# Kernel tuning notes

Hardware: AMD Instinct MI355X
Metric: run time of the kernel (lower is better)

## Reference

```python
import jax, jax.numpy as jnp
import numpy as np

B, S, D, H = 4, 1024, 2048, 16
DH = D // H          # head_dim = 128
EPS = 1e-6           # equinox nn.RMSNorm default eps


def setup_inputs() -> dict:
    ks = jax.random.split(jax.random.key(0), 8)
    return {
        "x": jax.random.normal(ks[0], (B, S, D), jnp.float32),
        # Flux-style rope table, broadcast over heads: (B, S, 1, d_head/2, 2, 2)
        "pe": jax.random.normal(ks[1], (B, S, 1, DH // 2, 2, 2), jnp.float32),
        "w_qkv": jax.random.normal(ks[2], (D, 3 * D), jnp.float32) * (1.0 / np.sqrt(D)),
        "w_o": jax.random.normal(ks[3], (D, D), jnp.float32) * (1.0 / np.sqrt(D)),
        "q_scale": 1.0 + 0.02 * jax.random.normal(ks[4], (DH,), jnp.float32),
        "q_bias": 0.02 * jax.random.normal(ks[5], (DH,), jnp.float32),
        "k_scale": 1.0 + 0.02 * jax.random.normal(ks[6], (DH,), jnp.float32),
        "k_bias": 0.02 * jax.random.normal(ks[7], (DH,), jnp.float32),
    }


def reference(x, pe, w_qkv, w_o, q_scale, q_bias, k_scale, k_bias):
    b, s, dm = x.shape
    # fused QKV projection -> (B, S, 3, H, DH); rearrange '(qkv heads dim)'
    qkv = (x @ w_qkv).reshape(b, s, 3, H, DH)
    q, k, v = qkv[:, :, 0], qkv[:, :, 1], qkv[:, :, 2]

    # per-head RMSNorm (QKNorm), eqx: w * (x / rms) + b
    def rms(u, scale, bias):
        inv = jax.lax.rsqrt(jnp.mean(u * u, axis=-1, keepdims=True) + EPS)
        return u * inv * scale + bias

    q = rms(q, q_scale, q_bias)
    k = rms(k, k_scale, k_bias)

    # RoPE: view last dim as (DH//2, 1, 2) pairs, apply 2x2 rotation from pe
    def rope(u):
        u2 = u.reshape(b, s, H, DH // 2, 1, 2)
        r = pe[..., 0] * u2[..., 0] + pe[..., 1] * u2[..., 1]  # (B,S,H,DH//2,2)
        return r.reshape(b, s, H, DH)

    q = rope(q)
    k = rope(k)

    # non-causal SDPA, layout (B, T, N, H), default scale 1/sqrt(DH)
    attn = jax.nn.dot_product_attention(q, k, v)
    return attn.reshape(b, s, dm) @ w_o
```

## Files before the change

kernel.cpp:

```cpp
#include <hip/hip_runtime.h>
#include <hip/hip_bf16.h>

typedef _Float16 f16_t;
typedef _Float16 f16x2 __attribute__((ext_vector_type(2)));
typedef _Float16 f16x4 __attribute__((ext_vector_type(4)));
typedef _Float16 f16x8 __attribute__((ext_vector_type(8)));
typedef float f32x4 __attribute__((ext_vector_type(4)));

#define GLOAD_LDS16(gp, lp)                                                        \
  __builtin_amdgcn_global_load_lds(                                                \
      (const __attribute__((address_space(1))) void*)(gp),                         \
      (__attribute__((address_space(3))) void*)(lp), 16, 0, 0)

template<int N> __device__ __forceinline__ void vmwait() {
    if constexpr (N == 0)      asm volatile("s_waitcnt vmcnt(0)" ::: "memory");
    else if constexpr (N == 3) asm volatile("s_waitcnt vmcnt(3)" ::: "memory");
    else if constexpr (N == 5) asm volatile("s_waitcnt vmcnt(5)" ::: "memory");
    else if constexpr (N == 6) asm volatile("s_waitcnt vmcnt(6)" ::: "memory");
    else                       asm volatile("s_waitcnt vmcnt(0)" ::: "memory");
}

__global__ __launch_bounds__(256) void conv_f16(const float* __restrict__ in,
                                                f16_t* __restrict__ out)
{
    int i = blockIdx.x * 256 + threadIdx.x;
    float4 a = *(const float4*)&in[(size_t)i * 8];
    float4 b = *(const float4*)&in[(size_t)i * 8 + 4];
    f16x8 o = {(f16_t)a.x, (f16_t)a.y, (f16_t)a.z, (f16_t)a.w,
               (f16_t)b.x, (f16_t)b.y, (f16_t)b.z, (f16_t)b.w};
    *(f16x8*)&out[(size_t)i * 8] = o;
}

__global__ __launch_bounds__(256) void transpose_f16(const float* __restrict__ in,
                                                     f16_t* __restrict__ out,
                                                     int R, int C)
{
    __shared__ float t[32][33];
    const int tr = blockIdx.y, tc = blockIdx.x;
    const int r = threadIdx.x >> 3, c4 = (threadIdx.x & 7) * 4;
    float4 v = *(const float4*)&in[(size_t)(tr * 32 + r) * C + tc * 32 + c4];
    t[r][c4 + 0] = v.x; t[r][c4 + 1] = v.y; t[r][c4 + 2] = v.z; t[r][c4 + 3] = v.w;
    __syncthreads();
    f16x4 o = {(f16_t)t[c4 + 0][r], (f16_t)t[c4 + 1][r],
               (f16_t)t[c4 + 2][r], (f16_t)t[c4 + 3][r]};
    *(f16x4*)&out[(size_t)(tc * 32 + r) * R + tr * 32 + c4] = o;
}

template<int BM, int BN, int GY, int F16OUT>
__global__ __launch_bounds__(512, 2) void gemm_v4(const f16_t* __restrict__ A,
                                                  const f16_t* __restrict__ BT,
                                                  void* __restrict__ Cout,
                                                  int M, int N, int K)
{
    extern __shared__ char smem[];
    constexpr int WMT = BM / 2, WNT = BN / 4;
    constexpr int MF = WMT / 16, NF = WNT / 16, MFH = MF / 2, NFH = NF / 2;
    constexpr int ALI = BM / 128, BLI = BN / 128;
    constexpr int L = ALI + BLI;
    constexpr int ABUFB = BM * 64, BBUFB = BN * 64;

    const int tid = threadIdx.x, lane = tid & 63, wave = tid >> 6;
    const int lh = lane >> 4, li = lane & 15;
    const int wr = wave >> 2, wc = wave & 3;

    const int nwg = gridDim.x, bid = blockIdx.x;
    const int swz = (bid & 7) * (nwg >> 3) + (bid >> 3);
    const int by = swz % GY, bx = swz / GY;

    const size_t bmK = (size_t)(by * BM) * K;
    const size_t bnK = (size_t)(bx * BN) * K;
    const int NT = K >> 5;

    f32x4 acc[MF][NF];
#pragma unroll
    for (int i = 0; i < MF; ++i)
#pragma unroll
        for (int j = 0; j < NF; ++j) acc[i][j] = (f32x4){0.f, 0.f, 0.f, 0.f};

#define STAGE(t, b)                                                                \
    do {                                                                           \
        const int kof_ = (t) << 5;                                                 \
        char* Ab_ = smem + (b) * ABUFB;                                            \
        char* Bb_ = smem + 3 * ABUFB + (b) * BBUFB;                                \
        _Pragma("unroll")                                                          \
        for (int i_ = 0; i_ < ALI; ++i_) {                                         \
            const int c_ = i_ * 512 + tid;                                         \
            const int row_ = c_ >> 2;                                              \
            const int gu_ = (c_ & 3) ^ ((row_ >> 1) & 3);                          \
            GLOAD_LDS16(A + bmK + (size_t)row_ * K + kof_ + gu_ * 8,               \
                        Ab_ + (i_ * 512 + wave * 64) * 16);                        \
        }                                                                          \
        _Pragma("unroll")                                                          \
        for (int i_ = 0; i_ < BLI; ++i_) {                                         \
            const int c_ = i_ * 512 + tid;                                         \
            const int row_ = c_ >> 2;                                              \
            const int gu_ = (c_ & 3) ^ ((row_ >> 1) & 3);                          \
            GLOAD_LDS16(BT + bnK + (size_t)row_ * K + kof_ + gu_ * 8,              \
                        Bb_ + (i_ * 512 + wave * 64) * 16);                        \
        }                                                                          \
    } while (0)

    STAGE(0, 0);
    STAGE(1, 1);

    const int runit = (lh ^ ((li >> 1) & 3)) << 3;

    int rb = 0;
    for (int t = 0; t < NT; ++t) {
        if (t + 1 < NT) vmwait<L>();
        else            vmwait<0>();
        __builtin_amdgcn_s_barrier();
        __builtin_amdgcn_sched_barrier(0);

        if (t + 2 < NT) {
            const int sb = rb ? rb - 1 : 2;
            STAGE(t + 2, sb);
        }

        const f16_t* Ab = (const f16_t*)(smem + rb * ABUFB);
        const f16_t* Bb = (const f16_t*)(smem + 3 * ABUFB + rb * BBUFB);

        f16x8 af[2][MFH], bf[NFH];
#pragma unroll
        for (int ah = 0; ah < 2; ++ah)
#pragma unroll
            for (int j = 0; j < MFH; ++j)
                af[ah][j] = *(const f16x8*)(Ab + (wr * WMT + (ah * MFH + j) * 16 + li) * 32
                                            + runit);
#pragma unroll
        for (int j = 0; j < NFH; ++j)
            bf[j] = *(const f16x8*)(Bb + (wc * WNT + j * 16 + li) * 32 + runit);

        __builtin_amdgcn_s_setprio(1);
#pragma unroll
        for (int ah = 0; ah < 2; ++ah)
#pragma unroll
            for (int i = 0; i < MFH; ++i)
#pragma unroll
                for (int j = 0; j < NFH; ++j)
                    acc[ah * MFH + i][j] = __builtin_amdgcn_mfma_f32_16x16x32_f16(
                        af[ah][i], bf[j], acc[ah * MFH + i][j], 0, 0, 0);
        __builtin_amdgcn_s_setprio(0);

#pragma unroll
        for (int j = 0; j < NFH; ++j)
            bf[j] = *(const f16x8*)(Bb + (wc * WNT + (NFH + j) * 16 + li) * 32 + runit);

        __builtin_amdgcn_s_setprio(1);
#pragma unroll
        for (int ah = 0; ah < 2; ++ah)
#pragma unroll
            for (int i = 0; i < MFH; ++i)
#pragma unroll
                for (int j = 0; j < NFH; ++j)
                    acc[ah * MFH + i][NFH + j] = __builtin_amdgcn_mfma_f32_16x16x32_f16(
                        af[ah][i], bf[j], acc[ah * MFH + i][NFH + j], 0, 0, 0);
        __builtin_amdgcn_s_setprio(0);

        __builtin_amdgcn_sched_barrier(0);
        rb = (rb == 2) ? 0 : rb + 1;
    }
#undef STAGE

#pragma unroll
    for (int mf = 0; mf < MF; ++mf)
#pragma unroll
        for (int nf = 0; nf < NF; ++nf)
#pragma unroll
            for (int r = 0; r < 4; ++r) {
                const int row = by * BM + wr * WMT + mf * 16 + lh * 4 + r;
                const int col = bx * BN + wc * WNT + nf * 16 + li;
                if (F16OUT)
                    ((f16_t*)Cout)[(size_t)row * N + col] = (f16_t)acc[mf][nf][r];
                else
                    ((float*)Cout)[(size_t)row * N + col] = acc[mf][nf][r];
            }
}

__global__ __launch_bounds__(256) void rmsrope_f16(f16_t* __restrict__ qkv,
                                                   const float* __restrict__ pe,
                                                   const float* __restrict__ qs,
                                                   const float* __restrict__ qb,
                                                   const float* __restrict__ ks,
                                                   const float* __restrict__ kb)
{
    const int unit = blockIdx.x * 4 + (threadIdx.x >> 6);
    const int l = threadIdx.x & 63;
    const int bs = unit >> 5, h = (unit >> 1) & 15, comp = unit & 1;
    f16_t* base = qkv + ((size_t)bs * 3 + comp) * 2048 + h * 128;
    const float* sc = comp ? ks : qs;
    const float* bi = comp ? kb : qb;

    f16x2 u = *(const f16x2*)(base + 2 * l);
    float u0 = (float)u[0], u1 = (float)u[1];
    float ss = u0 * u0 + u1 * u1;
#pragma unroll
    for (int o = 32; o; o >>= 1) ss += __shfl_xor(ss, o);
    float inv = rsqrtf(ss * (1.f / 128.f) + 1e-6f);

    float2 scv = *(const float2*)(sc + 2 * l);
    float2 biv = *(const float2*)(bi + 2 * l);
    float a = u0 * inv * scv.x + biv.x;
    float c = u1 * inv * scv.y + biv.y;
    float4 p4 = *(const float4*)(pe + (size_t)bs * 256 + l * 4);
    f16x2 o = {(f16_t)(p4.x * a + p4.y * c), (f16_t)(p4.z * a + p4.w * c)};
    *(f16x2*)(base + 2 * l) = o;
}

__global__ __launch_bounds__(256) void attn_f16(const f16_t* __restrict__ qkv,
                                                f16_t* __restrict__ out)
{
    __shared__ f16_t Kl[2][64 * 128];
    __shared__ f16_t Vt[128 * 72];
    const int tid = threadIdx.x, lane = tid & 63, wave = tid >> 6;
    const int lh = lane >> 4, li = lane & 15;
    const int bidx = blockIdx.x;
    const int bh = bidx & 63;
    const int qt = bidx >> 6;
    const int h = bh & 15, b = bh >> 4;
    const size_t seqbase = (size_t)b * 1024;
    const float SCALE = 0.08838834764831845f;

    const int qbase = qt * 128 + wave * 32;
    f16x8 qreg[2][4];
#pragma unroll
    for (int qf = 0; qf < 2; ++qf) {
        const f16_t* qp = qkv + (seqbase + qbase + qf * 16 + li) * 6144 + h * 128;
#pragma unroll
        for (int c = 0; c < 4; ++c) {
            f16x8 v = *(const f16x8*)(qp + c * 32 + lh * 8);
#pragma unroll
            for (int j = 0; j < 8; ++j) v[j] = (f16_t)((float)v[j] * SCALE);
            qreg[qf][c] = v;
        }
    }

    f32x4 oacc[2][8];
#pragma unroll
    for (int qf = 0; qf < 2; ++qf)
#pragma unroll
        for (int dt = 0; dt < 8; ++dt) oacc[qf][dt] = (f32x4){0.f, 0.f, 0.f, 0.f};
    float mrun[2] = {-1e30f, -1e30f}, lrun[2] = {0.f, 0.f};

    const int vd0 = (tid & 31) * 4;
    const int vk0 = (tid >> 5) * 8;
    f16x4 vreg[8];

#define STAGE_K(t, buf)                                                            \
    do {                                                                           \
        _Pragma("unroll")                                                          \
        for (int it = 0; it < 4; ++it) {                                           \
            const int c_ = it * 256 + tid;                                         \
            const int row_ = c_ >> 4, cc_ = c_ & 15;                               \
            const f16_t* src_ = qkv + (seqbase + (t) * 64 + row_) * 6144 + 2048 +  \
                                h * 128 + ((cc_ ^ (row_ & 7)) << 3);               \
            GLOAD_LDS16(src_, (char*)&Kl[buf][0] + (it * 256 + wave * 64) * 16);   \
        }                                                                          \
    } while (0)

#define LOAD_V(t)                                                                  \
    do {                                                                           \
        _Pragma("unroll")                                                          \
        for (int r_ = 0; r_ < 8; ++r_)                                             \
            vreg[r_] = *(const f16x4*)(qkv + (seqbase + (t) * 64 + vk0 + r_) *     \
                                       6144 + 4096 + h * 128 + vd0);               \
    } while (0)

    STAGE_K(0, 0);
    LOAD_V(0);

    for (int t = 0; t < 16; ++t) {
        const int buf = t & 1;
        __syncthreads();

#pragma unroll
        for (int dd = 0; dd < 4; ++dd) {
            f16x8 w;
#pragma unroll
            for (int r = 0; r < 8; ++r) w[r] = vreg[r][dd];
            *(f16x8*)&Vt[(vd0 + dd) * 72 + vk0] = w;
        }
        __syncthreads();

        if (t < 15) {
            STAGE_K(t + 1, buf ^ 1);
            LOAD_V(t + 1);
        }

        float s[2][16];
#pragma unroll
        for (int kvt = 0; kvt < 4; ++kvt) {
            f32x4 a0 = (f32x4){0.f, 0.f, 0.f, 0.f}, a1 = a0;
#pragma unroll
            for (int c = 0; c < 4; ++c) {
                const int kvrow = kvt * 16 + li;
                f16x8 kf = *(const f16x8*)&Kl[buf][kvrow * 128 +
                                                   (((c * 4 + lh) ^ (li & 7)) << 3)];
                a0 = __builtin_amdgcn_mfma_f32_16x16x32_f16(kf, qreg[0][c], a0, 0, 0, 0);
                a1 = __builtin_amdgcn_mfma_f32_16x16x32_f16(kf, qreg[1][c], a1, 0, 0, 0);
            }
#pragma unroll
            for (int r = 0; r < 4; ++r) { s[0][kvt * 4 + r] = a0[r]; s[1][kvt * 4 + r] = a1[r]; }
        }

        float pmax[2];
#pragma unroll
        for (int qf = 0; qf < 2; ++qf) {
            float mx = s[qf][0];
#pragma unroll
            for (int i = 1; i < 16; ++i) mx = fmaxf(mx, s[qf][i]);
            mx = fmaxf(mx, __shfl_xor(mx, 16));
            mx = fmaxf(mx, __shfl_xor(mx, 32));
            pmax[qf] = mx;
        }
        const bool defer = __all((pmax[0] - mrun[0] <= 8.f) && (pmax[1] - mrun[1] <= 8.f));
        if (!defer) {
#pragma unroll
            for (int qf = 0; qf < 2; ++qf) {
                const float mn = fmaxf(mrun[qf], pmax[qf]);
                const float alpha = __expf(mrun[qf] - mn);
                lrun[qf] *= alpha;
                mrun[qf] = mn;
                float ar[4];
#pragma unroll
                for (int r = 0; r < 4; ++r) ar[r] = __shfl(alpha, 4 * lh + r);
#pragma unroll
                for (int dt = 0; dt < 8; ++dt)
#pragma unroll
                    for (int r = 0; r < 4; ++r) oacc[qf][dt][r] *= ar[r];
            }
        }

        f16x8 pa[2][2];
#pragma unroll
        for (int qf = 0; qf < 2; ++qf) {
            float ls = 0.f;
            float p[16];
#pragma unroll
            for (int i = 0; i < 16; ++i) { p[i] = __expf(s[qf][i] - mrun[qf]); ls += p[i]; }
            ls += __shfl_xor(ls, 16);
            ls += __shfl_xor(ls, 32);
            lrun[qf] += ls;
#pragma unroll
            for (int hf = 0; hf < 2; ++hf)
#pragma unroll
                for (int j = 0; j < 8; ++j)
                    pa[qf][hf][j] = (f16_t)p[(2 * hf + (j >> 2)) * 4 + (j & 3)];
        }

#pragma unroll
        for (int dt = 0; dt < 8; ++dt) {
            const int drow = dt * 16 + li;
            f16x4 v0 = *(const f16x4*)&Vt[drow * 72 + 4 * lh];
            f16x4 v1 = *(const f16x4*)&Vt[drow * 72 + 16 + 4 * lh];
            f16x4 v2 = *(const f16x4*)&Vt[drow * 72 + 32 + 4 * lh];
            f16x4 v3 = *(const f16x4*)&Vt[drow * 72 + 48 + 4 * lh];
            f16x8 vf0 = {v0[0], v0[1], v0[2], v0[3], v1[0], v1[1], v1[2], v1[3]};
            f16x8 vf1 = {v2[0], v2[1], v2[2], v2[3], v3[0], v3[1], v3[2], v3[3]};
#pragma unroll
            for (int qf = 0; qf < 2; ++qf) {
                oacc[qf][dt] = __builtin_amdgcn_mfma_f32_16x16x32_f16(pa[qf][0], vf0,
                                                                      oacc[qf][dt], 0, 0, 0);
                oacc[qf][dt] = __builtin_amdgcn_mfma_f32_16x16x32_f16(pa[qf][1], vf1,
                                                                      oacc[qf][dt], 0, 0, 0);
            }
        }
    }

#pragma unroll
    for (int qf = 0; qf < 2; ++qf) {
        const float inv = 1.f / lrun[qf];
        float ir[4];
#pragma unroll
        for (int r = 0; r < 4; ++r) ir[r] = __shfl(inv, 4 * lh + r);
#pragma unroll
        for (int dt = 0; dt < 8; ++dt)
#pragma unroll
            for (int r = 0; r < 4; ++r) {
                const int row = qbase + qf * 16 + 4 * lh + r;
                out[(seqbase + row) * 2048 + h * 128 + dt * 16 + li] =
                    (f16_t)(oacc[qf][dt][r] * ir[r]);
            }
    }
#undef STAGE_K
#undef LOAD_V
}

extern "C" void kernel_launch(void* const* d_in, const int* in_sizes, int n_in,
                              void* d_out, int out_size, void* d_ws, size_t ws_size,
                              hipStream_t stream) {
    const float* x       = (const float*)d_in[0];
    const float* pe      = (const float*)d_in[1];
    const float* w_qkv   = (const float*)d_in[2];
    const float* w_o     = (const float*)d_in[3];
    const float* q_scale = (const float*)d_in[4];
    const float* q_bias  = (const float*)d_in[5];
    const float* k_scale = (const float*)d_in[6];
    const float* k_bias  = (const float*)d_in[7];
    float* out = (float*)d_out;

    char* ws = (char*)d_ws;
    f16_t* x16    = (f16_t*)(ws);
    f16_t* wqkvT  = (f16_t*)(ws + 16777216);
    f16_t* woT    = (f16_t*)(ws + 41943040);
    f16_t* qkv16  = (f16_t*)(ws + 50331648);
    f16_t* attn16 = (f16_t*)(ws + 100663296);

    hipFuncSetAttribute((const void*)&gemm_v4<256, 384, 16, 1>,
                        hipFuncAttributeMaxDynamicSharedMemorySize, 122880);
    hipFuncSetAttribute((const void*)&gemm_v4<128, 256, 32, 0>,
                        hipFuncAttributeMaxDynamicSharedMemorySize, 73728);

    conv_f16<<<4096, 256, 0, stream>>>(x, x16);
    transpose_f16<<<dim3(6144 / 32, 2048 / 32), 256, 0, stream>>>(w_qkv, wqkvT, 2048, 6144);
    transpose_f16<<<dim3(2048 / 32, 2048 / 32), 256, 0, stream>>>(w_o, woT, 2048, 2048);

    gemm_v4<256, 384, 16, 1><<<256, 512, 122880, stream>>>(x16, wqkvT, qkv16,
                                                           4096, 6144, 2048);

    rmsrope_f16<<<32768, 256, 0, stream>>>(qkv16, pe, q_scale, q_bias, k_scale, k_bias);

    attn_f16<<<512, 256, 0, stream>>>(qkv16, attn16);

    gemm_v4<128, 256, 32, 0><<<256, 512, 73728, stream>>>(attn16, woT, out,
                                                          4096, 2048, 2048);
}
```

Measured before the change: 273.8 us.

## Split GEMM main loop into four barrier-synced phases interleaving LDS reads and staging

Restructures the GEMM k-loop into four MFMA phases separated by workgroup barriers, interleaving LDS fragment reads with split A/B global-to-LDS staging so memory issue and matrix math from different waves overlap in a ping-pong style. The wait for the next tile moves to the end of the iteration, with a prologue wait before the loop. This adds three extra barriers per k-step in exchange for better overlap. Buffer reuse safety relies on the three-buffer rotation and barrier placement.

```diff
diff --git a/kernel.cpp b/kernel.cpp
--- a/kernel.cpp
+++ b/kernel.cpp
@@ -16,9 +16,15 @@
     if constexpr (N == 0)      asm volatile("s_waitcnt vmcnt(0)" ::: "memory");
     else if constexpr (N == 3) asm volatile("s_waitcnt vmcnt(3)" ::: "memory");
     else if constexpr (N == 5) asm volatile("s_waitcnt vmcnt(5)" ::: "memory");
-    else if constexpr (N == 6) asm volatile("s_waitcnt vmcnt(6)" ::: "memory");
     else                       asm volatile("s_waitcnt vmcnt(0)" ::: "memory");
 }
+
+#define PHASE_SYNC()                                                               \
+    do {                                                                           \
+        __builtin_amdgcn_s_barrier();                                              \
+        asm volatile("s_waitcnt lgkmcnt(0)" ::: "memory");                         \
+        __builtin_amdgcn_sched_barrier(0);                                         \
+    } while (0)
 
 __global__ __launch_bounds__(256) void conv_f16(const float* __restrict__ in,
                                                 f16_t* __restrict__ out)
@@ -47,7 +53,7 @@
 }
 
 template<int BM, int BN, int GY, int F16OUT>
-__global__ __launch_bounds__(512, 2) void gemm_v4(const f16_t* __restrict__ A,
+__global__ __launch_bounds__(512, 2) void gemm_v7(const f16_t* __restrict__ A,
                                                   const f16_t* __restrict__ BT,
                                                   void* __restrict__ Cout,
                                                   int M, int N, int K)
@@ -77,11 +83,10 @@
 #pragma unroll
         for (int j = 0; j < NF; ++j) acc[i][j] = (f32x4){0.f, 0.f, 0.f, 0.f};
 
-#define STAGE(t, b)                                                                \
+#define STAGE_A(t, b)                                                              \
     do {                                                                           \
         const int kof_ = (t) << 5;                                                 \
         char* Ab_ = smem + (b) * ABUFB;                                            \
-        char* Bb_ = smem + 3 * ABUFB + (b) * BBUFB;                                \
         _Pragma("unroll")                                                          \
         for (int i_ = 0; i_ < ALI; ++i_) {                                         \
             const int c_ = i_ * 512 + tid;                                         \
@@ -90,6 +95,12 @@
             GLOAD_LDS16(A + bmK + (size_t)row_ * K + kof_ + gu_ * 8,               \
                         Ab_ + (i_ * 512 + wave * 64) * 16);                        \
         }                                                                          \
+    } while (0)
+
+#define STAGE_B(t, b)                                                              \
+    do {                                                                           \
+        const int kof_ = (t) << 5;                                                 \
+        char* Bb_ = smem + 3 * ABUFB + (b) * BBUFB;                                \
         _Pragma("unroll")                                                          \
         for (int i_ = 0; i_ < BLI; ++i_) {                                         \
             const int c_ = i_ * 512 + tid;                                         \
@@ -100,67 +111,85 @@
         }                                                                          \
     } while (0)
 
-    STAGE(0, 0);
-    STAGE(1, 1);
+    STAGE_A(0, 0); STAGE_B(0, 0);
+    STAGE_A(1, 1); STAGE_B(1, 1);
+    vmwait<L>();
+    __builtin_amdgcn_s_barrier();
+    __builtin_amdgcn_sched_barrier(0);
 
     const int runit = (lh ^ ((li >> 1) & 3)) << 3;
 
     int rb = 0;
     for (int t = 0; t < NT; ++t) {
-        if (t + 1 < NT) vmwait<L>();
-        else            vmwait<0>();
+        const f16_t* Ab = (const f16_t*)(smem + rb * ABUFB);
+        const f16_t* Bb = (const f16_t*)(smem + 3 * ABUFB + rb * BBUFB);
+        const int sb = rb ? rb - 1 : 2;
+        const bool stg = (t + 2 < NT);
+
+        f16x8 af[2][MFH], bf[NFH];
+
+#pragma unroll
+        for (int j = 0; j < MFH; ++j)
+            af[0][j] = *(const f16x8*)(Ab + (wr * WMT + j * 16 + li) * 32 + runit);
+#pragma unroll
+        for (int j = 0; j < NFH; ++j)
+            bf[j] = *(const f16x8*)(Bb + (wc * WNT + j * 16 + li) * 32 + runit);
+        if (stg) STAGE_A(t + 2, sb);
+        PHASE_SYNC();
+        __builtin_amdgcn_s_setprio(1);
+#pragma unroll
+        for (int i = 0; i < MFH; ++i)
+#pragma unroll
+            for (int j = 0; j < NFH; ++j)
+                acc[i][j] = __builtin_amdgcn_mfma_f32_16x16x32_f16(af[0][i], bf[j],
+                                                                   acc[i][j], 0, 0, 0);
+        __builtin_amdgcn_s_setprio(0);
+
+#pragma unroll
+        for (int j = 0; j < MFH; ++j)
+            af[1][j] = *(const f16x8*)(Ab + (wr * WMT + (MFH + j) * 16 + li) * 32 + runit);
+        if (stg) STAGE_B(t + 2, sb);
+        PHASE_SYNC();
+        __builtin_amdgcn_s_setprio(1);
+#pragma unroll
+        for (int i = 0; i < MFH; ++i)
+#pragma unroll
+            for (int j = 0; j < NFH; ++j)
+                acc[MFH + i][j] = __builtin_amdgcn_mfma_f32_16x16x32_f16(af[1][i], bf[j],
+                                                                         acc[MFH + i][j],
+                                                                         0, 0, 0);
+        __builtin_amdgcn_s_setprio(0);
+
+#pragma unroll
+        for (int j = 0; j < NFH; ++j)
+            bf[j] = *(const f16x8*)(Bb + (wc * WNT + (NFH + j) * 16 + li) * 32 + runit);
+        PHASE_SYNC();
+        __builtin_amdgcn_s_setprio(1);
+#pragma unroll
+        for (int i = 0; i < MFH; ++i)
+#pragma unroll
+            for (int j = 0; j < NFH; ++j)
+                acc[MFH + i][NFH + j] = __builtin_amdgcn_mfma_f32_16x16x32_f16(
+                    af[1][i], bf[j], acc[MFH + i][NFH + j], 0, 0, 0);
+        __builtin_amdgcn_s_setprio(0);
+
+        if (stg) vmwait<L>();
+        else     vmwait<0>();
         __builtin_amdgcn_s_barrier();
         __builtin_amdgcn_sched_barrier(0);
-
-        if (t + 2 < NT) {
-            const int sb = rb ? rb - 1 : 2;
-            STAGE(t + 2, sb);
-        }
-
-        const f16_t* Ab = (const f16_t*)(smem + rb * ABUFB);
-        const f16_t* Bb = (const f16_t*)(smem + 3 * ABUFB + rb * BBUFB);
-
-        f16x8 af[2][MFH], bf[NFH];
-#pragma unroll
-        for (int ah = 0; ah < 2; ++ah)
-#pragma unroll
-            for (int j = 0; j < MFH; ++j)
-                af[ah][j] = *(const f16x8*)(Ab + (wr * WMT + (ah * MFH + j) * 16 + li) * 32
-                                            + runit);
-#pragma unroll
-        for (int j = 0; j < NFH; ++j)
-            bf[j] = *(const f16x8*)(Bb + (wc * WNT + j * 16 + li) * 32 + runit);
-
         __builtin_amdgcn_s_setprio(1);
 #pragma unroll
-        for (int ah = 0; ah < 2; ++ah)
-#pragma unroll
-            for (int i = 0; i < MFH; ++i)
-#pragma unroll
-                for (int j = 0; j < NFH; ++j)
-                    acc[ah * MFH + i][j] = __builtin_amdgcn_mfma_f32_16x16x32_f16(
-                        af[ah][i], bf[j], acc[ah * MFH + i][j], 0, 0, 0);
+        for (int i = 0; i < MFH; ++i)
+#pragma unroll
+            for (int j = 0; j < NFH; ++j)
+                acc[i][NFH + j] = __builtin_amdgcn_mfma_f32_16x16x32_f16(
+                    af[0][i], bf[j], acc[i][NFH + j], 0, 0, 0);
         __builtin_amdgcn_s_setprio(0);
 
-#pragma unroll
-        for (int j = 0; j < NFH; ++j)
-            bf[j] = *(const f16x8*)(Bb + (wc * WNT + (NFH + j) * 16 + li) * 32 + runit);
-
-        __builtin_amdgcn_s_setprio(1);
-#pragma unroll
-        for (int ah = 0; ah < 2; ++ah)
-#pragma unroll
-            for (int i = 0; i < MFH; ++i)
-#pragma unroll
-                for (int j = 0; j < NFH; ++j)
-                    acc[ah * MFH + i][NFH + j] = __builtin_amdgcn_mfma_f32_16x16x32_f16(
-                        af[ah][i], bf[j], acc[ah * MFH + i][NFH + j], 0, 0, 0);
-        __builtin_amdgcn_s_setprio(0);
-
-        __builtin_amdgcn_sched_barrier(0);
         rb = (rb == 2) ? 0 : rb + 1;
     }
-#undef STAGE
+#undef STAGE_A
+#undef STAGE_B
 
 #pragma unroll
     for (int mf = 0; mf < MF; ++mf)
@@ -406,22 +435,22 @@
     f16_t* qkv16  = (f16_t*)(ws + 50331648);
     f16_t* attn16 = (f16_t*)(ws + 100663296);
 
-    hipFuncSetAttribute((const void*)&gemm_v4<256, 384, 16, 1>,
+    hipFuncSetAttribute((const void*)&gemm_v7<256, 384, 16, 1>,
                         hipFuncAttributeMaxDynamicSharedMemorySize, 122880);
-    hipFuncSetAttribute((const void*)&gemm_v4<128, 256, 32, 0>,
+    hipFuncSetAttribute((const void*)&gemm_v7<128, 256, 32, 0>,
                         hipFuncAttributeMaxDynamicSharedMemorySize, 73728);
 
     conv_f16<<<4096, 256, 0, stream>>>(x, x16);
     transpose_f16<<<dim3(6144 / 32, 2048 / 32), 256, 0, stream>>>(w_qkv, wqkvT, 2048, 6144);
     transpose_f16<<<dim3(2048 / 32, 2048 / 32), 256, 0, stream>>>(w_o, woT, 2048, 2048);
 
-    gemm_v4<256, 384, 16, 1><<<256, 512, 122880, stream>>>(x16, wqkvT, qkv16,
+    gemm_v7<256, 384, 16, 1><<<256, 512, 122880, stream>>>(x16, wqkvT, qkv16,
                                                            4096, 6144, 2048);
 
     rmsrope_f16<<<32768, 256, 0, stream>>>(qkv16, pe, q_scale, q_bias, k_scale, k_bias);
 
     attn_f16<<<512, 256, 0, stream>>>(qkv16, attn16);
 
-    gemm_v4<128, 256, 32, 0><<<256, 512, 73728, stream>>>(attn16, woT, out,
+    gemm_v7<128, 256, 32, 0><<<256, 512, 73728, stream>>>(attn16, woT, out,
                                                           4096, 2048, 2048);
 }
```

After: 295.0 us. 1.08x slower.

## Double-buffer V tile with swizzled layout and reschedule attention loop syncs

Applied to the files above, without the earlier changes.

The attention kernel now double-buffers the transposed V tile in dynamic shared memory and uses an XOR-swizzled layout, so each P·V operand becomes a single 16-byte LDS read instead of four 8-byte reads. The next tile's V is written at the end of each iteration, which cuts the two barriers per iteration to one and lets the QK^T MFMAs start right away. It also raises wave priority around the MFMA blocks. In exchange, LDS use grows to about 68 KB, which may reduce how many blocks fit per CU, and a full vmcnt wait before the V write can stall.

```diff
diff --git a/kernel.cpp b/kernel.cpp
--- a/kernel.cpp
+++ b/kernel.cpp
@@ -16,7 +16,6 @@
     if constexpr (N == 0)      asm volatile("s_waitcnt vmcnt(0)" ::: "memory");
     else if constexpr (N == 3) asm volatile("s_waitcnt vmcnt(3)" ::: "memory");
     else if constexpr (N == 5) asm volatile("s_waitcnt vmcnt(5)" ::: "memory");
-    else if constexpr (N == 6) asm volatile("s_waitcnt vmcnt(6)" ::: "memory");
     else                       asm volatile("s_waitcnt vmcnt(0)" ::: "memory");
 }
 
@@ -210,8 +209,9 @@
 __global__ __launch_bounds__(256) void attn_f16(const f16_t* __restrict__ qkv,
                                                 f16_t* __restrict__ out)
 {
-    __shared__ f16_t Kl[2][64 * 128];
-    __shared__ f16_t Vt[128 * 72];
+    extern __shared__ char asmem[];
+    f16_t* KlP = (f16_t*)asmem;
+    f16_t* VtP = (f16_t*)(asmem + 32768);
     const int tid = threadIdx.x, lane = tid & 63, wave = tid >> 6;
     const int lh = lane >> 4, li = lane & 15;
     const int bidx = blockIdx.x;
@@ -243,7 +243,8 @@
     float mrun[2] = {-1e30f, -1e30f}, lrun[2] = {0.f, 0.f};
 
     const int vd0 = (tid & 31) * 4;
-    const int vk0 = (tid >> 5) * 8;
+    const int w5 = tid >> 5;
+    const int vk0 = w5 * 8;
     f16x4 vreg[8];
 
 #define STAGE_K(t, buf)                                                            \
@@ -254,7 +255,8 @@
             const int row_ = c_ >> 4, cc_ = c_ & 15;                               \
             const f16_t* src_ = qkv + (seqbase + (t) * 64 + row_) * 6144 + 2048 +  \
                                 h * 128 + ((cc_ ^ (row_ & 7)) << 3);               \
-            GLOAD_LDS16(src_, (char*)&Kl[buf][0] + (it * 256 + wave * 64) * 16);   \
+            GLOAD_LDS16(src_, (char*)KlP + (buf) * 16384 +                         \
+                        (it * 256 + wave * 64) * 16);                              \
         }                                                                          \
     } while (0)
 
@@ -266,41 +268,52 @@
                                        6144 + 4096 + h * 128 + vd0);               \
     } while (0)
 
+#define WRITE_VT(bufv)                                                             \
+    do {                                                                           \
+        const int u0_ = 4 * (w5 & 1) + (w5 >> 2);                                  \
+        const int woff_ = 4 * ((w5 >> 1) & 1);                                     \
+        _Pragma("unroll")                                                          \
+        for (int dd = 0; dd < 4; ++dd) {                                           \
+            const int rr_ = vd0 + dd;                                              \
+            const int xr_ = (rr_ & 7) ^ ((rr_ >> 3) & 7);                          \
+            f16x4 wv0 = {vreg[0][dd], vreg[1][dd], vreg[2][dd], vreg[3][dd]};      \
+            f16x4 wv1 = {vreg[4][dd], vreg[5][dd], vreg[6][dd], vreg[7][dd]};      \
+            f16_t* bp_ = VtP + (bufv) * 9216 + rr_ * 72;                           \
+            *(f16x4*)(bp_ + ((u0_ ^ xr_) << 3) + woff_) = wv0;                     \
+            *(f16x4*)(bp_ + (((u0_ + 2) ^ xr_) << 3) + woff_) = wv1;               \
+        }                                                                          \
+    } while (0)
+
     STAGE_K(0, 0);
     LOAD_V(0);
+    asm volatile("s_waitcnt vmcnt(0)" ::: "memory");
+    WRITE_VT(0);
+    __syncthreads();
 
     for (int t = 0; t < 16; ++t) {
         const int buf = t & 1;
-        __syncthreads();
-
-#pragma unroll
-        for (int dd = 0; dd < 4; ++dd) {
-            f16x8 w;
-#pragma unroll
-            for (int r = 0; r < 8; ++r) w[r] = vreg[r][dd];
-            *(f16x8*)&Vt[(vd0 + dd) * 72 + vk0] = w;
-        }
-        __syncthreads();
+
+        float s[2][16];
+#pragma unroll
+        for (int kvt = 0; kvt < 4; ++kvt) {
+            f32x4 a0 = (f32x4){0.f, 0.f, 0.f, 0.f}, a1 = a0;
+            __builtin_amdgcn_s_setprio(1);
+#pragma unroll
+            for (int c = 0; c < 4; ++c) {
+                const int kvrow = kvt * 16 + li;
+                f16x8 kf = *(const f16x8*)&KlP[buf * 8192 + kvrow * 128 +
+                                               (((c * 4 + lh) ^ (li & 7)) << 3)];
+                a0 = __builtin_amdgcn_mfma_f32_16x16x32_f16(kf, qreg[0][c], a0, 0, 0, 0);
+                a1 = __builtin_amdgcn_mfma_f32_16x16x32_f16(kf, qreg[1][c], a1, 0, 0, 0);
+            }
+            __builtin_amdgcn_s_setprio(0);
+#pragma unroll
+            for (int r = 0; r < 4; ++r) { s[0][kvt * 4 + r] = a0[r]; s[1][kvt * 4 + r] = a1[r]; }
+        }
 
         if (t < 15) {
             STAGE_K(t + 1, buf ^ 1);
             LOAD_V(t + 1);
-        }
-
-        float s[2][16];
-#pragma unroll
-        for (int kvt = 0; kvt < 4; ++kvt) {
-            f32x4 a0 = (f32x4){0.f, 0.f, 0.f, 0.f}, a1 = a0;
-#pragma unroll
-            for (int c = 0; c < 4; ++c) {
-                const int kvrow = kvt * 16 + li;
-                f16x8 kf = *(const f16x8*)&Kl[buf][kvrow * 128 +
-                                                   (((c * 4 + lh) ^ (li & 7)) << 3)];
-                a0 = __builtin_amdgcn_mfma_f32_16x16x32_f16(kf, qreg[0][c], a0, 0, 0, 0);
-                a1 = __builtin_amdgcn_mfma_f32_16x16x32_f16(kf, qreg[1][c], a1, 0, 0, 0);
-            }
-#pragma unroll
-            for (int r = 0; r < 4; ++r) { s[0][kvt * 4 + r] = a0[r]; s[1][kvt * 4 + r] = a1[r]; }
         }
 
         float pmax[2];
@@ -351,12 +364,11 @@
 #pragma unroll
         for (int dt = 0; dt < 8; ++dt) {
             const int drow = dt * 16 + li;
-            f16x4 v0 = *(const f16x4*)&Vt[drow * 72 + 4 * lh];
-            f16x4 v1 = *(const f16x4*)&Vt[drow * 72 + 16 + 4 * lh];
-            f16x4 v2 = *(const f16x4*)&Vt[drow * 72 + 32 + 4 * lh];
-            f16x4 v3 = *(const f16x4*)&Vt[drow * 72 + 48 + 4 * lh];
-            f16x8 vf0 = {v0[0], v0[1], v0[2], v0[3], v1[0], v1[1], v1[2], v1[3]};
-            f16x8 vf1 = {v2[0], v2[1], v2[2], v2[3], v3[0], v3[1], v3[2], v3[3]};
+            const int xr = (drow & 7) ^ ((drow >> 3) & 7);
+            const f16_t* bp = VtP + buf * 9216 + drow * 72;
+            f16x8 vf0 = *(const f16x8*)(bp + (((lh * 2) ^ xr) << 3));
+            f16x8 vf1 = *(const f16x8*)(bp + (((lh * 2 + 1) ^ xr) << 3));
+            __builtin_amdgcn_s_setprio(1);
 #pragma unroll
             for (int qf = 0; qf < 2; ++qf) {
                 oacc[qf][dt] = __builtin_amdgcn_mfma_f32_16x16x32_f16(pa[qf][0], vf0,
@@ -364,6 +376,13 @@
                 oacc[qf][dt] = __builtin_amdgcn_mfma_f32_16x16x32_f16(pa[qf][1], vf1,
                                                                       oacc[qf][dt], 0, 0, 0);
             }
+            __builtin_amdgcn_s_setprio(0);
+        }
+
+        if (t < 15) {
+            asm volatile("s_waitcnt vmcnt(0)" ::: "memory");
+            WRITE_VT(buf ^ 1);
+            __syncthreads();
         }
     }
 
@@ -384,6 +403,7 @@
     }
 #undef STAGE_K
 #undef LOAD_V
+#undef WRITE_VT
 }
 
 extern "C" void kernel_launch(void* const* d_in, const int* in_sizes, int n_in,
@@ -410,6 +430,8 @@
                         hipFuncAttributeMaxDynamicSharedMemorySize, 122880);
     hipFuncSetAttribute((const void*)&gemm_v4<128, 256, 32, 0>,
                         hipFuncAttributeMaxDynamicSharedMemorySize, 73728);
+    hipFuncSetAttribute((const void*)&attn_f16,
+                        hipFuncAttributeMaxDynamicSharedMemorySize, 69632);
 
     conv_f16<<<4096, 256, 0, stream>>>(x, x16);
     transpose_f16<<<dim3(6144 / 32, 2048 / 32), 256, 0, stream>>>(w_qkv, wqkvT, 2048, 6144);
@@ -420,7 +442,7 @@
 
     rmsrope_f16<<<32768, 256, 0, stream>>>(qkv16, pe, q_scale, q_bias, k_scale, k_bias);
 
-    attn_f16<<<512, 256, 0, stream>>>(qkv16, attn16);
+    attn_f16<<<512, 256, 69632, stream>>>(qkv16, attn16);
 
     gemm_v4<128, 256, 32, 0><<<256, 512, 73728, stream>>>(attn16, woT, out,
                                                           4096, 2048, 2048);
```

Result: faster. 260.7 us (-4.8%).
